# Kernel tuning notes

Hardware: AMD Instinct MI355X
Metric: run time of the kernel (lower is better)

## Reference

```python
import jax, jax.numpy as jnp
import numpy as np

N_NODES = 100000
N_EDGES = 1600000
F_IN = 128
F_OUT = 64
BN_EPS = 1e-5


def setup_inputs() -> dict:
    key = jax.random.key(0)
    k1, k2, k3, k4, k5, k6 = jax.random.split(key, 6)
    x = jax.random.normal(k1, (N_NODES, F_IN), dtype=jnp.float32)
    edge_index = jax.random.randint(k2, (2, N_EDGES), 0, N_NODES, dtype=jnp.int64)
    edge_weight = jax.random.uniform(k3, (N_EDGES,), dtype=jnp.float32)
    # learned params: linear weight (no bias), batchnorm gamma/beta
    W = jax.random.normal(k4, (F_OUT, F_IN), dtype=jnp.float32) * (1.0 / np.sqrt(F_IN))
    gamma = jnp.ones((F_OUT,), dtype=jnp.float32)
    beta = jnp.zeros((F_OUT,), dtype=jnp.float32)
    return {"x": x, "edge_index": edge_index, "edge_weight": edge_weight,
            "W": W, "gamma": gamma, "beta": beta}


def reference(x, edge_index, edge_weight, W, gamma, beta):
    N = x.shape[0]
    h = x @ W.T  # [N, F_OUT]
    # add self loops with weight 1.0
    loop = jnp.arange(N, dtype=edge_index.dtype)
    src = jnp.concatenate([edge_index[0], loop])
    dst = jnp.concatenate([edge_index[1], loop])
    w = jnp.concatenate([edge_weight, jnp.ones((N,), dtype=h.dtype)])
    # degree of row (src) counts edge occurrences (unweighted)
    deg = jax.ops.segment_sum(jnp.ones_like(w), src, num_segments=N)
    dinv = jnp.where(deg > 0, jax.lax.rsqrt(deg), 0.0)
    norm = dinv[src] * w * dinv[dst]  # [E+N]
    # gather-scale-scatter aggregation
    out = jax.ops.segment_sum(h[src] * norm[:, None], dst, num_segments=N)
    out = jax.nn.relu(out)
    # BatchNorm1d (training mode: biased batch stats over nodes)
    mean = jnp.mean(out, axis=0)
    var = jnp.mean((out - mean) ** 2, axis=0)
    out = (out - mean) * jax.lax.rsqrt(var + BN_EPS) * gamma + beta
    # dropout p=0.0 -> identity
    return out
```

## Files before the change

kernel.cpp:

```cpp
#include <hip/hip_runtime.h>

#define N_NODES 100000
#define N_EDGES 1600000
#define F_IN 128
#define F_OUT 64
#define BN_EPS 1e-5f

#define NPART 2
#define NCHUNK 128
#define PSIZE 50000
#define CHUNK_E 12500

#define SCAN_NB 98


typedef __attribute__((ext_vector_type(8))) short bf16x8;
typedef __attribute__((ext_vector_type(4))) float f32x4;

__device__ __forceinline__ unsigned short f2bf(float x) {
    unsigned u = __float_as_uint(x);
    u += 0x7fffu + ((u >> 16) & 1u);
    return (unsigned short)(u >> 16);
}
__device__ __forceinline__ float4 bf4(uint2 p) {
    return make_float4(__int_as_float((int)(p.x << 16)),
                       __int_as_float((int)(p.x & 0xffff0000u)),
                       __int_as_float((int)(p.y << 16)),
                       __int_as_float((int)(p.y & 0xffff0000u)));
}

__global__ __launch_bounds__(512) void count_kernel(const void* __restrict__ ei,
                                                    int* __restrict__ s32,
                                                    int* __restrict__ d32,
                                                    unsigned* __restrict__ partial32) {
    __shared__ unsigned bins[PSIZE / 4];
    const long long* q = (const long long*)ei;
    long long probe = q[threadIdx.x & 63];
    bool badp = (probe < 0 || probe >= N_NODES);
    int is64 = (__ballot(badp) == 0ULL);

    const int tid = threadIdx.x;
    const int p = blockIdx.x % NPART;
    const int b = blockIdx.x / NPART;
    const int p0 = p * PSIZE;
    for (int i = tid; i < PSIZE / 4; i += 512) bins[i] = 0u;
    __syncthreads();
    const int e0 = b * CHUNK_E;
    for (int i = tid; i < CHUNK_E / 4; i += 512) {
        int e = e0 + i * 4;
        int4 s, d;
        if (is64) {
            longlong2 a = *(const longlong2*)&q[e];
            longlong2 bb = *(const longlong2*)&q[e + 2];
            s = make_int4((int)a.x, (int)a.y, (int)bb.x, (int)bb.y);
            longlong2 c2 = *(const longlong2*)&q[N_EDGES + e];
            longlong2 e2 = *(const longlong2*)&q[N_EDGES + e + 2];
            d = make_int4((int)c2.x, (int)c2.y, (int)e2.x, (int)e2.y);
        } else {
            s = ((const int4*)ei)[e >> 2];
            d = ((const int4*)ei)[(N_EDGES >> 2) + (e >> 2)];
        }
        if (p == 0) ((int4*)s32)[e >> 2] = s;
#define C1(sk, dk, kk) { \
        unsigned si = (unsigned)((sk) - p0); \
        if (si < PSIZE) atomicAdd(&bins[si >> 2], 1u << ((si & 3) * 8)); \
        unsigned dd = (unsigned)((dk) - p0); \
        if ((unsigned)(sk) < N_NODES && dd < PSIZE) { \
            unsigned sh = (dd & 3) * 8 + 4; \
            unsigned old = atomicAdd(&bins[dd >> 2], 16u << ((dd & 3) * 8)); \
            d32[e + kk] = (dk) | (int)(((old >> sh) & 0xFu) << 27); } }
        C1(s.x, d.x, 0) C1(s.y, d.y, 1) C1(s.z, d.z, 2) C1(s.w, d.w, 3)
#undef C1
    }
    __syncthreads();
    unsigned* dst = partial32 + (unsigned)blockIdx.x * (PSIZE / 4);
    for (int i = tid; i < PSIZE / 4; i += 512) dst[i] = bins[i];
}

__global__ __launch_bounds__(256) void redscan_kernel(unsigned* __restrict__ partial32,
                                                      float* __restrict__ dinv,
                                                      unsigned* __restrict__ off,
                                                      unsigned* __restrict__ bsum,
                                                      float* __restrict__ sums) {
    __shared__ unsigned s[256];
    const int tid = threadIdx.x;
    if (blockIdx.x == 0 && tid < 128) sums[tid] = 0.f;
    const int n0 = blockIdx.x * 1024 + tid * 4;
    unsigned cntk[4] = {0, 0, 0, 0};
    unsigned degk[4] = {0, 0, 0, 0};
    if (n0 < N_NODES) {
        unsigned idx = (unsigned)n0 >> 2;
#pragma unroll 8
        for (int c = 0; c < NCHUNK; ++c) {
            unsigned v = partial32[idx];
            unsigned nv = 0;
#pragma unroll
            for (int k = 0; k < 4; ++k) {
                unsigned byte = (v >> (k * 8)) & 0xFFu;
                nv |= (cntk[k] & 0xFFu) << (k * 8);
                cntk[k] += byte >> 4;
                degk[k] += byte & 0xFu;
            }
            partial32[idx] = nv;
            idx += (NPART * PSIZE) / 4;
        }
#pragma unroll
        for (int k = 0; k < 4; ++k)
            dinv[n0 + k] = rsqrtf((float)(degk[k] + 1u));
    }
    unsigned tsum = cntk[0] + cntk[1] + cntk[2] + cntk[3];
    s[tid] = tsum;
    __syncthreads();
    for (int d = 1; d < 256; d <<= 1) {
        unsigned t = (tid >= d) ? s[tid - d] : 0u;
        __syncthreads();
        s[tid] += t;
        __syncthreads();
    }
    unsigned run = s[tid] - tsum;
    if (n0 < N_NODES) {
        uint4 o;
        o.x = run;
        o.y = run + cntk[0];
        o.z = o.y + cntk[1];
        o.w = o.z + cntk[2];
        *(uint4*)&off[n0] = o;
    }
    if (tid == 255) bsum[blockIdx.x] = s[255];
}

__global__ __launch_bounds__(128) void scan2_kernel(unsigned* __restrict__ bsum) {
    __shared__ unsigned s[128];
    const int tid = threadIdx.x;
    unsigned v = (tid < SCAN_NB) ? bsum[tid] : 0u;
    s[tid] = v;
    __syncthreads();
    for (int d = 1; d < 128; d <<= 1) {
        unsigned t = (tid >= d) ? s[tid - d] : 0u;
        __syncthreads();
        s[tid] += t;
        __syncthreads();
    }
    if (tid < SCAN_NB) bsum[tid] = s[tid] - v;
}

__global__ __launch_bounds__(256) void place_kernel(const int* __restrict__ s32,
                                                    const int* __restrict__ d32,
                                                    const float* __restrict__ ew,
                                                    const unsigned* __restrict__ off,
                                                    const unsigned* __restrict__ bsum,
                                                    const unsigned* __restrict__ partial32,
                                                    int2* __restrict__ buck) {
    int i = blockIdx.x * 256 + threadIdx.x;
    if (i >= N_EDGES / 4) return;
    int4 s = ((const int4*)s32)[i];
    int4 d = ((const int4*)d32)[i];
    float4 w = ((const float4*)ew)[i];
    const unsigned char* pb = (const unsigned char*)partial32;
    int e = i * 4;
    int b = e / CHUNK_E;
    unsigned base = (unsigned)b * NPART * PSIZE;
#define P1(sk, dvk, wk) { \
    unsigned dd = (unsigned)(dvk) & 0x07FFFFFFu; \
    unsigned rk = ((unsigned)(dvk)) >> 27; \
    if ((unsigned)(sk) < N_NODES && dd < N_NODES) { \
        unsigned pref = pb[base + dd]; \
        unsigned slot = off[dd] + bsum[dd >> 10] + pref + rk; \
        if (slot < N_EDGES) \
            buck[slot] = make_int2((sk), __float_as_int(wk)); } }
    P1(s.x, d.x, w.x) P1(s.y, d.y, w.y) P1(s.z, d.z, w.z) P1(s.w, d.w, w.w)
#undef P1
}

__global__ __launch_bounds__(256) void gemm_kernel(const float* __restrict__ x,
                                                   const float* __restrict__ W,
                                                   const float* __restrict__ dinv,
                                                   unsigned short* __restrict__ hb) {
    __shared__ short wlds[16 * 64 * 8];
    const int tid = threadIdx.x;
    const int n0 = blockIdx.x * 64;
    {
        int out = tid & 63;
        int kb = tid >> 6;
#pragma unroll
        for (int i = 0; i < 4; ++i) {
            int koct = kb + i * 4;
            const float* wp = &W[out * F_IN + koct * 8];
            float4 aa = *(const float4*)wp;
            float4 bb = *(const float4*)(wp + 4);
            bf16x8 f;
            f[0] = (short)f2bf(aa.x); f[1] = (short)f2bf(aa.y);
            f[2] = (short)f2bf(aa.z); f[3] = (short)f2bf(aa.w);
            f[4] = (short)f2bf(bb.x); f[5] = (short)f2bf(bb.y);
            f[6] = (short)f2bf(bb.z); f[7] = (short)f2bf(bb.w);
            ((bf16x8*)wlds)[koct * 64 + out] = f;
        }
    }
    __syncthreads();
    const int wv = tid >> 6;
    const int lane = tid & 63;
    const int m = lane & 15;
    const int quad = lane >> 4;
    const int row = n0 + wv * 16 + m;
    const bool rv = row < N_NODES;
    const float* xrow = &x[(long)row * F_IN + quad * 8];
    f32x4 acc0 = {0.f, 0.f, 0.f, 0.f};
    f32x4 acc1 = {0.f, 0.f, 0.f, 0.f};
    f32x4 acc2 = {0.f, 0.f, 0.f, 0.f};
    f32x4 acc3 = {0.f, 0.f, 0.f, 0.f};
#pragma unroll
    for (int kc = 0; kc < 4; ++kc) {
        bf16x8 a = {0, 0, 0, 0, 0, 0, 0, 0};
        if (rv) {
            float4 aa = *(const float4*)(xrow + kc * 32);
            float4 bb = *(const float4*)(xrow + kc * 32 + 4);
            a[0] = (short)f2bf(aa.x); a[1] = (short)f2bf(aa.y);
            a[2] = (short)f2bf(aa.z); a[3] = (short)f2bf(aa.w);
            a[4] = (short)f2bf(bb.x); a[5] = (short)f2bf(bb.y);
            a[6] = (short)f2bf(bb.z); a[7] = (short)f2bf(bb.w);
        }
        const bf16x8* wrow = &((const bf16x8*)wlds)[(kc * 4 + quad) * 64 + m];
        acc0 = __builtin_amdgcn_mfma_f32_16x16x32_bf16(a, wrow[0],  acc0, 0, 0, 0);
        acc1 = __builtin_amdgcn_mfma_f32_16x16x32_bf16(a, wrow[16], acc1, 0, 0, 0);
        acc2 = __builtin_amdgcn_mfma_f32_16x16x32_bf16(a, wrow[32], acc2, 0, 0, 0);
        acc3 = __builtin_amdgcn_mfma_f32_16x16x32_bf16(a, wrow[48], acc3, 0, 0, 0);
    }
#pragma unroll
    for (int r = 0; r < 4; ++r) {
        int node = n0 + wv * 16 + quad * 4 + r;
        if (node < N_NODES) {
            float dv = dinv[node];
            unsigned short* hr = &hb[(long)node * F_OUT + m];
            hr[0]  = f2bf(acc0[r] * dv);
            hr[16] = f2bf(acc1[r] * dv);
            hr[32] = f2bf(acc2[r] * dv);
            hr[48] = f2bf(acc3[r] * dv);
        }
    }
}

#define AGG_BLOCKS 2048
#define NPW 13
__global__ __launch_bounds__(256) void aggregate_kernel(
    const unsigned short* __restrict__ hb, const float* __restrict__ dinv,
    const unsigned* __restrict__ off, const unsigned* __restrict__ bsum,
    const int2* __restrict__ buck, float* __restrict__ out,
    float* __restrict__ sums) {
    const int tid = threadIdx.x;
    const int wv = tid >> 6;
    const int lane = tid & 63;
    const int es = lane >> 4;
    const int cl = lane & 15;
    float s1[4] = {0.f, 0.f, 0.f, 0.f};
    float s2[4] = {0.f, 0.f, 0.f, 0.f};

    const int wid = blockIdx.x * 4 + wv;
    const int nbeg = wid * NPW;
    const int nend = (nbeg + NPW < N_NODES) ? nbeg + NPW : N_NODES;
    for (int n = nbeg; n < nend; ++n) {
        const unsigned o = off[n] + bsum[(unsigned)n >> 10];
        const unsigned onext = (n + 1 < N_NODES)
            ? off[n + 1] + bsum[(unsigned)(n + 1) >> 10]
            : (unsigned)N_EDGES;
        const unsigned c = onext - o;
        float4 a0 = make_float4(0.f, 0.f, 0.f, 0.f);
        float4 a1 = make_float4(0.f, 0.f, 0.f, 0.f);
        unsigned j = es;
        for (; j + 4 < c; j += 8) {
            int2 b1 = buck[o + j];
            int2 b2 = buck[o + j + 4];
            float4 h1 = bf4(((const uint2*)(hb + ((long)b1.x << 6)))[cl]);
            float4 h2 = bf4(((const uint2*)(hb + ((long)b2.x << 6)))[cl]);
            float w1 = __int_as_float(b1.y);
            float w2 = __int_as_float(b2.y);
            a0.x += h1.x * w1; a0.y += h1.y * w1; a0.z += h1.z * w1; a0.w += h1.w * w1;
            a1.x += h2.x * w2; a1.y += h2.y * w2; a1.z += h2.z * w2; a1.w += h2.w * w2;
        }
        if (j < c) {
            int2 bb = buck[o + j];
            float w = __int_as_float(bb.y);
            float4 hv = bf4(((const uint2*)(hb + ((long)bb.x << 6)))[cl]);
            a0.x += hv.x * w; a0.y += hv.y * w; a0.z += hv.z * w; a0.w += hv.w * w;
        }
        a0.x += a1.x; a0.y += a1.y; a0.z += a1.z; a0.w += a1.w;
        a0.x += __shfl_xor(a0.x, 16); a0.y += __shfl_xor(a0.y, 16);
        a0.z += __shfl_xor(a0.z, 16); a0.w += __shfl_xor(a0.w, 16);
        a0.x += __shfl_xor(a0.x, 32); a0.y += __shfl_xor(a0.y, 32);
        a0.z += __shfl_xor(a0.z, 32); a0.w += __shfl_xor(a0.w, 32);
        if (es == 0) {
            float dn = dinv[n];
            float4 hn = bf4(((const uint2*)(hb + ((long)n << 6)))[cl]);
            a0.x = fmaxf(dn * (a0.x + hn.x), 0.f);
            a0.y = fmaxf(dn * (a0.y + hn.y), 0.f);
            a0.z = fmaxf(dn * (a0.z + hn.z), 0.f);
            a0.w = fmaxf(dn * (a0.w + hn.w), 0.f);
            *(float4*)&out[(long)n * F_OUT + cl * 4] = a0;
            s1[0] += a0.x; s1[1] += a0.y; s1[2] += a0.z; s1[3] += a0.w;
            s2[0] += a0.x * a0.x; s2[1] += a0.y * a0.y;
            s2[2] += a0.z * a0.z; s2[3] += a0.w * a0.w;
        }
    }
    __shared__ float l1[256];
    __shared__ float l2[256];
    if (es == 0) {
#pragma unroll
        for (int k = 0; k < 4; ++k) {
            l1[wv * 64 + cl * 4 + k] = s1[k];
            l2[wv * 64 + cl * 4 + k] = s2[k];
        }
    }
    __syncthreads();
    if (tid < 64) {
        float b1 = l1[tid] + l1[64 + tid] + l1[128 + tid] + l1[192 + tid];
        float b2 = l2[tid] + l2[64 + tid] + l2[128 + tid] + l2[192 + tid];
        atomicAdd(&sums[tid], b1);
        atomicAdd(&sums[64 + tid], b2);
    }
}

__global__ __launch_bounds__(256) void apply_kernel(float* __restrict__ agg,
                                                    const float* __restrict__ sums,
                                                    const float* __restrict__ gamma,
                                                    const float* __restrict__ beta) {
    __shared__ float sc[64], bi[64];
    if (threadIdx.x < 64) {
        int c = threadIdx.x;
        const float inv_n = 1.0f / (float)N_NODES;
        float mean = sums[c] * inv_n;
        float var = sums[64 + c] * inv_n - mean * mean;
        float rs = rsqrtf(var + BN_EPS);
        float scale = rs * gamma[c];
        sc[c] = scale;
        bi[c] = beta[c] - mean * scale;
    }
    __syncthreads();
    int i = blockIdx.x * blockDim.x + threadIdx.x;
    if (i >= N_NODES * 16) return;
    int c4 = (i & 15) << 2;
    float4 v = ((float4*)agg)[i];
    v.x = v.x * sc[c4 + 0] + bi[c4 + 0];
    v.y = v.y * sc[c4 + 1] + bi[c4 + 1];
    v.z = v.z * sc[c4 + 2] + bi[c4 + 2];
    v.w = v.w * sc[c4 + 3] + bi[c4 + 3];
    ((float4*)agg)[i] = v;
}

extern "C" void kernel_launch(void* const* d_in, const int* in_sizes, int n_in,
                              void* d_out, int out_size, void* d_ws, size_t ws_size,
                              hipStream_t stream) {
    const float* x     = (const float*)d_in[0];
    const void*  ei    = d_in[1];
    const float* ew    = (const float*)d_in[2];
    const float* W     = (const float*)d_in[3];
    const float* gamma = (const float*)d_in[4];
    const float* beta  = (const float*)d_in[5];
    float* out = (float*)d_out;
    float* ws  = (float*)d_ws;

    int*            s32       = (int*)ws;
    int*            d32       = (int*)(ws + 1600000);
    unsigned*       partial32 = (unsigned*)(ws + 3200000);
    unsigned short* hb        = (unsigned short*)(ws + 3200000);
    int2*           buck      = (int2*)(ws + 6400000);
    float*          dinv      = ws + 9600000;
    float*          sums      = ws + 9700000;
    unsigned*       off       = (unsigned*)(ws + 9800128);
    unsigned*       bsum      = (unsigned*)(ws + 9900128);

    count_kernel<<<NPART * NCHUNK, 512, 0, stream>>>(ei, s32, d32, partial32);
    redscan_kernel<<<SCAN_NB, 256, 0, stream>>>(partial32, dinv, off, bsum, sums);
    scan2_kernel<<<1, 128, 0, stream>>>(bsum);
    place_kernel<<<(N_EDGES / 4 + 255) / 256, 256, 0, stream>>>(s32, d32, ew, off, bsum,
                                                                partial32, buck);
    gemm_kernel<<<(N_NODES + 63) / 64, 256, 0, stream>>>(x, W, dinv, hb);
    aggregate_kernel<<<AGG_BLOCKS, 256, 0, stream>>>(hb, dinv, off, bsum, buck, out, sums);
    apply_kernel<<<(N_NODES * 16 + 255) / 256, 256, 0, stream>>>(out, sums, gamma, beta);
}
```

Measured before the change: 291.6 us.

## Software-pipeline bucket index loads across nodes in aggregation kernel

```diff
diff --git a/kernel.cpp b/kernel.cpp
--- a/kernel.cpp
+++ b/kernel.cpp
@@ -241,6 +241,13 @@
 
 #define AGG_BLOCKS 2048
 #define NPW 13
+
+#define ACC4(A, P, W) { \
+    A[0] += __int_as_float((int)((P).x << 16)) * (W); \
+    A[1] += __int_as_float((int)((P).x & 0xffff0000u)) * (W); \
+    A[2] += __int_as_float((int)((P).y << 16)) * (W); \
+    A[3] += __int_as_float((int)((P).y & 0xffff0000u)) * (W); }
+
 __global__ __launch_bounds__(256) void aggregate_kernel(
     const unsigned short* __restrict__ hb, const float* __restrict__ dinv,
     const unsigned* __restrict__ off, const unsigned* __restrict__ bsum,
@@ -257,48 +264,72 @@
     const int wid = blockIdx.x * 4 + wv;
     const int nbeg = wid * NPW;
     const int nend = (nbeg + NPW < N_NODES) ? nbeg + NPW : N_NODES;
+
+    unsigned o = 0;
+    int2 pb0 = make_int2(0, 0), pb1 = make_int2(0, 0);
+    if (nbeg < nend) {
+        o = off[nbeg] + bsum[(unsigned)nbeg >> 10];
+        unsigned a0 = o + (unsigned)es;
+        unsigned a1 = o + (unsigned)es + 4u;
+        if (a0 > (unsigned)(N_EDGES - 1)) a0 = (unsigned)(N_EDGES - 1);
+        if (a1 > (unsigned)(N_EDGES - 1)) a1 = (unsigned)(N_EDGES - 1);
+        pb0 = buck[a0];
+        pb1 = buck[a1];
+    }
+    uint2 pg0 = make_uint2(0u, 0u), pg1 = make_uint2(0u, 0u);
+    float pw0 = 0.f, pw1 = 0.f;
+
     for (int n = nbeg; n < nend; ++n) {
-        const unsigned o = off[n] + bsum[(unsigned)n >> 10];
         const unsigned onext = (n + 1 < N_NODES)
             ? off[n + 1] + bsum[(unsigned)(n + 1) >> 10]
             : (unsigned)N_EDGES;
         const unsigned c = onext - o;
-        float4 a0 = make_float4(0.f, 0.f, 0.f, 0.f);
-        float4 a1 = make_float4(0.f, 0.f, 0.f, 0.f);
-        unsigned j = es;
-        for (; j + 4 < c; j += 8) {
-            int2 b1 = buck[o + j];
-            int2 b2 = buck[o + j + 4];
-            float4 h1 = bf4(((const uint2*)(hb + ((long)b1.x << 6)))[cl]);
-            float4 h2 = bf4(((const uint2*)(hb + ((long)b2.x << 6)))[cl]);
-            float w1 = __int_as_float(b1.y);
-            float w2 = __int_as_float(b2.y);
-            a0.x += h1.x * w1; a0.y += h1.y * w1; a0.z += h1.z * w1; a0.w += h1.w * w1;
-            a1.x += h2.x * w2; a1.y += h2.y * w2; a1.z += h2.z * w2; a1.w += h2.w * w2;
-        }
-        if (j < c) {
-            int2 bb = buck[o + j];
-            float w = __int_as_float(bb.y);
-            float4 hv = bf4(((const uint2*)(hb + ((long)bb.x << 6)))[cl]);
-            a0.x += hv.x * w; a0.y += hv.y * w; a0.z += hv.z * w; a0.w += hv.w * w;
-        }
-        a0.x += a1.x; a0.y += a1.y; a0.z += a1.z; a0.w += a1.w;
-        a0.x += __shfl_xor(a0.x, 16); a0.y += __shfl_xor(a0.y, 16);
-        a0.z += __shfl_xor(a0.z, 16); a0.w += __shfl_xor(a0.w, 16);
-        a0.x += __shfl_xor(a0.x, 32); a0.y += __shfl_xor(a0.y, 32);
-        a0.z += __shfl_xor(a0.z, 32); a0.w += __shfl_xor(a0.w, 32);
+        const uint2 hn = ((const uint2*)(hb + ((long)n << 6)))[cl];
+        const float dn = dinv[n];
+        float acc[4] = {0.f, 0.f, 0.f, 0.f};
+        const int nb = (int)((c + 7u) >> 3);
+        bool pend = false;
+        for (int k = 0; k < nb; ++k) {
+            const unsigned jb = (unsigned)k * 8u;
+            const bool v0 = (jb + (unsigned)es) < c;
+            const bool v1 = (jb + (unsigned)es + 4u) < c;
+            const int2 b0 = pb0;
+            const int2 b1 = pb1;
+            unsigned r0 = (unsigned)b0.x; if (r0 > (unsigned)(N_NODES - 1)) r0 = 0u;
+            unsigned r1 = (unsigned)b1.x; if (r1 > (unsigned)(N_NODES - 1)) r1 = 0u;
+            const uint2 g0 = ((const uint2*)(hb + ((long)r0 << 6)))[cl];
+            const uint2 g1 = ((const uint2*)(hb + ((long)r1 << 6)))[cl];
+            const float w0 = v0 ? __int_as_float(b0.y) : 0.f;
+            const float w1 = v1 ? __int_as_float(b1.y) : 0.f;
+            const unsigned base = (k + 1 < nb) ? (o + jb + 8u) : onext;
+            unsigned a0 = base + (unsigned)es;
+            unsigned a1 = base + (unsigned)es + 4u;
+            if (a0 > (unsigned)(N_EDGES - 1)) a0 = (unsigned)(N_EDGES - 1);
+            if (a1 > (unsigned)(N_EDGES - 1)) a1 = (unsigned)(N_EDGES - 1);
+            pb0 = buck[a0];
+            pb1 = buck[a1];
+            if (pend) { ACC4(acc, pg0, pw0) ACC4(acc, pg1, pw1) }
+            pg0 = g0; pg1 = g1; pw0 = w0; pw1 = w1;
+            pend = true;
+        }
+        if (pend) { ACC4(acc, pg0, pw0) ACC4(acc, pg1, pw1) }
+#pragma unroll
+        for (int k = 0; k < 4; ++k) {
+            acc[k] += __shfl_xor(acc[k], 16);
+            acc[k] += __shfl_xor(acc[k], 32);
+        }
         if (es == 0) {
-            float dn = dinv[n];
-            float4 hn = bf4(((const uint2*)(hb + ((long)n << 6)))[cl]);
-            a0.x = fmaxf(dn * (a0.x + hn.x), 0.f);
-            a0.y = fmaxf(dn * (a0.y + hn.y), 0.f);
-            a0.z = fmaxf(dn * (a0.z + hn.z), 0.f);
-            a0.w = fmaxf(dn * (a0.w + hn.w), 0.f);
-            *(float4*)&out[(long)n * F_OUT + cl * 4] = a0;
-            s1[0] += a0.x; s1[1] += a0.y; s1[2] += a0.z; s1[3] += a0.w;
-            s2[0] += a0.x * a0.x; s2[1] += a0.y * a0.y;
-            s2[2] += a0.z * a0.z; s2[3] += a0.w * a0.w;
-        }
+            float4 hv = bf4(hn);
+            float r0 = fmaxf(dn * (acc[0] + hv.x), 0.f);
+            float r1 = fmaxf(dn * (acc[1] + hv.y), 0.f);
+            float r2 = fmaxf(dn * (acc[2] + hv.z), 0.f);
+            float r3 = fmaxf(dn * (acc[3] + hv.w), 0.f);
+            *(float4*)&out[(long)n * F_OUT + cl * 4] = make_float4(r0, r1, r2, r3);
+            s1[0] += r0; s1[1] += r1; s1[2] += r2; s1[3] += r3;
+            s2[0] += r0 * r0; s2[1] += r1 * r1;
+            s2[2] += r2 * r2; s2[3] += r3 * r3;
+        }
+        o = onext;
     }
     __shared__ float l1[256];
     __shared__ float l2[256];
```

Result: faster. 281.7 us (-3.4%).

## Software-pipeline aggregate gathers across node boundaries in a flat edge stream

Applied to the files above, without the earlier changes.

```diff
diff --git a/kernel.cpp b/kernel.cpp
--- a/kernel.cpp
+++ b/kernel.cpp
@@ -241,6 +241,66 @@
 
 #define AGG_BLOCKS 2048
 #define NPW 13
+
+#define ACC4(A, P, W) { \
+    A[0] += __int_as_float((int)((P).x << 16)) * (W); \
+    A[1] += __int_as_float((int)((P).x & 0xffff0000u)) * (W); \
+    A[2] += __int_as_float((int)((P).y << 16)) * (W); \
+    A[3] += __int_as_float((int)((P).y & 0xffff0000u)) * (W); }
+
+#define LOADB(B0_, B1_, QV) { \
+    unsigned a0_ = (QV) + (unsigned)es; \
+    unsigned a1_ = a0_ + 4u; \
+    if (a0_ > (unsigned)(N_EDGES - 1)) a0_ = (unsigned)(N_EDGES - 1); \
+    if (a1_ > (unsigned)(N_EDGES - 1)) a1_ = (unsigned)(N_EDGES - 1); \
+    B0_ = buck[a0_]; B1_ = buck[a1_]; }
+
+#define GISSUE(G0_, G1_, W0_, W1_, B0_, B1_) { \
+    unsigned r0_ = (unsigned)(B0_).x; if (r0_ > (unsigned)(N_NODES - 1)) r0_ = 0u; \
+    unsigned r1_ = (unsigned)(B1_).x; if (r1_ > (unsigned)(N_NODES - 1)) r1_ = 0u; \
+    G0_ = ((const uint2*)(hb + ((long)r0_ << 6)))[cl]; \
+    G1_ = ((const uint2*)(hb + ((long)r1_ << 6)))[cl]; \
+    W0_ = __int_as_float((B0_).y); W1_ = __int_as_float((B1_).y); }
+
+#define FIN() { \
+    acc[0] += __shfl_xor(acc[0], 16); acc[1] += __shfl_xor(acc[1], 16); \
+    acc[2] += __shfl_xor(acc[2], 16); acc[3] += __shfl_xor(acc[3], 16); \
+    acc[0] += __shfl_xor(acc[0], 32); acc[1] += __shfl_xor(acc[1], 32); \
+    acc[2] += __shfl_xor(acc[2], 32); acc[3] += __shfl_xor(acc[3], 32); \
+    if (es == 0) { \
+        float4 hv = bf4(hn); \
+        float r0_ = fmaxf(dn * (acc[0] + hv.x), 0.f); \
+        float r1_ = fmaxf(dn * (acc[1] + hv.y), 0.f); \
+        float r2_ = fmaxf(dn * (acc[2] + hv.z), 0.f); \
+        float r3_ = fmaxf(dn * (acc[3] + hv.w), 0.f); \
+        int node_ = nbeg + ncur; \
+        *(float4*)&out[(long)node_ * F_OUT + cl * 4] = make_float4(r0_, r1_, r2_, r3_); \
+        s1[0] += r0_; s1[1] += r1_; s1[2] += r2_; s1[3] += r3_; \
+        s2[0] += r0_ * r0_; s2[1] += r1_ * r1_; \
+        s2[2] += r2_ * r2_; s2[3] += r3_ * r3_; \
+    } \
+    acc[0] = acc[1] = acc[2] = acc[3] = 0.f; \
+    ++ncur; \
+    if (ncur < nn) { \
+        seg_lo = bnd; \
+        bnd = __shfl(bl, ncur + 1); \
+        dn = __shfl(dvl, ncur); \
+        hn = ((const uint2*)(hb + ((long)(nbeg + ncur) << 6)))[cl]; \
+    } else { seg_lo = 0xFFFFFFFFu; bnd = 0xFFFFFFFFu; } }
+
+#define CONSUME(G0_, G1_, W0_, W1_, QV) { \
+    const unsigned qc_ = (QV); \
+    const unsigned p0_ = qc_ + (unsigned)es; \
+    const unsigned p1_ = p0_ + 4u; \
+    for (;;) { \
+        float m0_ = (p0_ >= seg_lo && p0_ < bnd) ? (W0_) : 0.f; \
+        float m1_ = (p1_ >= seg_lo && p1_ < bnd) ? (W1_) : 0.f; \
+        ACC4(acc, G0_, m0_) ACC4(acc, G1_, m1_) \
+        if (bnd > qc_ + 8u) break; \
+        FIN() \
+        if (seg_lo >= qc_ + 8u) break; \
+    } }
+
 __global__ __launch_bounds__(256) void aggregate_kernel(
     const unsigned short* __restrict__ hb, const float* __restrict__ dinv,
     const unsigned* __restrict__ off, const unsigned* __restrict__ bsum,
@@ -253,53 +313,66 @@
     const int cl = lane & 15;
     float s1[4] = {0.f, 0.f, 0.f, 0.f};
     float s2[4] = {0.f, 0.f, 0.f, 0.f};
+    float acc[4] = {0.f, 0.f, 0.f, 0.f};
 
     const int wid = blockIdx.x * 4 + wv;
     const int nbeg = wid * NPW;
-    const int nend = (nbeg + NPW < N_NODES) ? nbeg + NPW : N_NODES;
-    for (int n = nbeg; n < nend; ++n) {
-        const unsigned o = off[n] + bsum[(unsigned)n >> 10];
-        const unsigned onext = (n + 1 < N_NODES)
-            ? off[n + 1] + bsum[(unsigned)(n + 1) >> 10]
-            : (unsigned)N_EDGES;
-        const unsigned c = onext - o;
-        float4 a0 = make_float4(0.f, 0.f, 0.f, 0.f);
-        float4 a1 = make_float4(0.f, 0.f, 0.f, 0.f);
-        unsigned j = es;
-        for (; j + 4 < c; j += 8) {
-            int2 b1 = buck[o + j];
-            int2 b2 = buck[o + j + 4];
-            float4 h1 = bf4(((const uint2*)(hb + ((long)b1.x << 6)))[cl]);
-            float4 h2 = bf4(((const uint2*)(hb + ((long)b2.x << 6)))[cl]);
-            float w1 = __int_as_float(b1.y);
-            float w2 = __int_as_float(b2.y);
-            a0.x += h1.x * w1; a0.y += h1.y * w1; a0.z += h1.z * w1; a0.w += h1.w * w1;
-            a1.x += h2.x * w2; a1.y += h2.y * w2; a1.z += h2.z * w2; a1.w += h2.w * w2;
-        }
-        if (j < c) {
-            int2 bb = buck[o + j];
-            float w = __int_as_float(bb.y);
-            float4 hv = bf4(((const uint2*)(hb + ((long)bb.x << 6)))[cl]);
-            a0.x += hv.x * w; a0.y += hv.y * w; a0.z += hv.z * w; a0.w += hv.w * w;
-        }
-        a0.x += a1.x; a0.y += a1.y; a0.z += a1.z; a0.w += a1.w;
-        a0.x += __shfl_xor(a0.x, 16); a0.y += __shfl_xor(a0.y, 16);
-        a0.z += __shfl_xor(a0.z, 16); a0.w += __shfl_xor(a0.w, 16);
-        a0.x += __shfl_xor(a0.x, 32); a0.y += __shfl_xor(a0.y, 32);
-        a0.z += __shfl_xor(a0.z, 32); a0.w += __shfl_xor(a0.w, 32);
-        if (es == 0) {
-            float dn = dinv[n];
-            float4 hn = bf4(((const uint2*)(hb + ((long)n << 6)))[cl]);
-            a0.x = fmaxf(dn * (a0.x + hn.x), 0.f);
-            a0.y = fmaxf(dn * (a0.y + hn.y), 0.f);
-            a0.z = fmaxf(dn * (a0.z + hn.z), 0.f);
-            a0.w = fmaxf(dn * (a0.w + hn.w), 0.f);
-            *(float4*)&out[(long)n * F_OUT + cl * 4] = a0;
-            s1[0] += a0.x; s1[1] += a0.y; s1[2] += a0.z; s1[3] += a0.w;
-            s2[0] += a0.x * a0.x; s2[1] += a0.y * a0.y;
-            s2[2] += a0.z * a0.z; s2[3] += a0.w * a0.w;
-        }
-    }
+    int nn = N_NODES - nbeg;
+    if (nn > NPW) nn = NPW;
+    if (nn < 0) nn = 0;
+
+    unsigned bl = (unsigned)N_EDGES;
+    float dvl = 0.f;
+    if (nn > 0) {
+        int n = nbeg + lane;
+        if (lane <= nn)
+            bl = (n < N_NODES) ? off[n] + bsum[(unsigned)n >> 10] : (unsigned)N_EDGES;
+        if (lane < nn) dvl = dinv[n];
+    }
+
+    if (nn > 0) {
+        const unsigned obeg = __shfl(bl, 0);
+        const unsigned oend = __shfl(bl, nn);
+        int ncur = 0;
+        unsigned seg_lo = obeg;
+        unsigned bnd = __shfl(bl, 1);
+        float dn = __shfl(dvl, 0);
+        uint2 hn = ((const uint2*)(hb + ((long)nbeg << 6)))[cl];
+
+        const int NB = (int)((oend - obeg + 7u) >> 3);
+        const int NB3 = ((NB + 2) / 3) * 3;
+
+        int2 b00, b01, b10, b11, b20, b21;
+        uint2 gA0, gA1, gB0, gB1, gC0, gC1;
+        float wA0, wA1, wB0, wB1, wC0, wC1;
+
+        if (NB3 > 0) {
+            LOADB(b00, b01, obeg)
+            LOADB(b10, b11, obeg + 8u)
+            LOADB(b20, b21, obeg + 16u)
+            GISSUE(gA0, gA1, wA0, wA1, b00, b01) LOADB(b00, b01, obeg + 24u)
+            GISSUE(gB0, gB1, wB0, wB1, b10, b11) LOADB(b10, b11, obeg + 32u)
+            GISSUE(gC0, gC1, wC0, wC1, b20, b21) LOADB(b20, b21, obeg + 40u)
+
+            for (int k = 3; k < NB3; k += 3) {
+                const unsigned q = obeg + ((unsigned)k << 3);
+                CONSUME(gA0, gA1, wA0, wA1, q - 24u)
+                GISSUE(gA0, gA1, wA0, wA1, b00, b01) LOADB(b00, b01, q + 24u)
+                CONSUME(gB0, gB1, wB0, wB1, q - 16u)
+                GISSUE(gB0, gB1, wB0, wB1, b10, b11) LOADB(b10, b11, q + 32u)
+                CONSUME(gC0, gC1, wC0, wC1, q - 8u)
+                GISSUE(gC0, gC1, wC0, wC1, b20, b21) LOADB(b20, b21, q + 40u)
+            }
+            {
+                const unsigned qd = obeg + ((unsigned)NB3 << 3);
+                CONSUME(gA0, gA1, wA0, wA1, qd - 24u)
+                CONSUME(gB0, gB1, wB0, wB1, qd - 16u)
+                CONSUME(gC0, gC1, wC0, wC1, qd - 8u)
+            }
+        }
+        while (ncur < nn) { FIN() }
+    }
+
     __shared__ float l1[256];
     __shared__ float l2[256];
     if (es == 0) {
```

Measured after the change: 277.8 us. -4.7%, faster.
